# Optimization experiments

Measured on AMD Instinct MI355X. Metric: run time of the kernel, lower is better.

The kernel has to match this reference:

```python
import jax, jax.numpy as jnp
import numpy as np

N_NODES = 100_000
N_EDGES = 1_600_000
VOCAB = 10_000
NUM_GRAPHS = 512
D_EMB, D_HID, D_OUT = 64, 128, 64


def _sage_conv(h, src, dst, Wl, b, Wr, num_nodes):
    """PyG SAGEConv with mean aggregation: lin_l(mean_{j in N(i)} x_j) + lin_r(x_i)."""
    msgs = h[src]                                               # [E, D]
    agg = jax.ops.segment_sum(msgs, dst, num_segments=num_nodes)
    deg = jax.ops.segment_sum(jnp.ones((src.shape[0], 1), h.dtype), dst,
                              num_segments=num_nodes)
    agg = agg / jnp.maximum(deg, 1.0)                           # mean over neighbors
    return agg @ Wl + b + h @ Wr


def setup_inputs() -> dict:
    key = jax.random.key(0)
    ks = jax.random.split(key, 12)
    x = jax.random.randint(ks[0], (N_NODES,), 0, VOCAB)
    edge_index = jax.random.randint(ks[1], (2, N_EDGES), 0, N_NODES)
    batch = jnp.sort(jax.random.randint(ks[2], (N_NODES,), 0, NUM_GRAPHS))
    edge_attr = jax.random.uniform(ks[3], (N_EDGES, 1), dtype=jnp.float32)
    embed = jax.random.normal(ks[4], (VOCAB, D_EMB), dtype=jnp.float32) * 0.02
    W1l = jax.random.normal(ks[5], (D_EMB, D_HID), dtype=jnp.float32) / np.sqrt(D_EMB)
    b1 = jnp.zeros((D_HID,), jnp.float32)
    W1r = jax.random.normal(ks[6], (D_EMB, D_HID), dtype=jnp.float32) / np.sqrt(D_EMB)
    W2l = jax.random.normal(ks[7], (D_HID, D_OUT), dtype=jnp.float32) / np.sqrt(D_HID)
    b2 = jnp.zeros((D_OUT,), jnp.float32)
    W2r = jax.random.normal(ks[8], (D_HID, D_OUT), dtype=jnp.float32) / np.sqrt(D_HID)
    return {"x": x, "edge_index": edge_index, "batch": batch, "edge_attr": edge_attr,
            "embed": embed, "W1l": W1l, "b1": b1, "W1r": W1r,
            "W2l": W2l, "b2": b2, "W2r": W2r}


def reference(x, edge_index, batch, edge_attr, embed, W1l, b1, W1r, W2l, b2, W2r):
    # edge_attr is passed in the original forward but PyG SAGEConv ignores edge weights.
    src, dst = edge_index[0], edge_index[1]
    h = embed[x]                                                # [N, 64]
    h = jax.nn.relu(_sage_conv(h, src, dst, W1l, b1, W1r, N_NODES))  # [N, 128]
    h = _sage_conv(h, src, dst, W2l, b2, W2r, N_NODES)          # [N, 64]
    out = jax.ops.segment_max(h, batch, num_segments=NUM_GRAPHS)  # [G, 64]
    return out
```

## Files before the change

### kernel.cpp

```cpp
#include <hip/hip_runtime.h>
#include <cstdint>

#define NN 100000
#define NE 1600000
#define NG 512
#define NP 100032
#define VOCAB 10000
#define NBUK 256
#define BSZ 391
#define CAP 7680
#define TILE 2048

typedef unsigned short u16;
typedef u16      u16x8  __attribute__((ext_vector_type(8)));
typedef __bf16   bf16x8 __attribute__((ext_vector_type(8)));
typedef float    f32x4  __attribute__((ext_vector_type(4)));
typedef float    f32x2  __attribute__((ext_vector_type(2)));
typedef unsigned uint4v __attribute__((ext_vector_type(4)));

__device__ __forceinline__ u16 f2bf(float f) {
    unsigned u = __float_as_uint(f);
    unsigned r = ((u >> 16) & 1u) + 0x7FFFu;
    return (u16)((u + r) >> 16);
}
__device__ __forceinline__ float bf2f(u16 h) {
    return __uint_as_float(((unsigned)h) << 16);
}

__device__ __forceinline__ unsigned encF(float f) {
    unsigned s = __float_as_uint(f);
    return (s & 0x80000000u) ? ~s : (s | 0x80000000u);
}
__device__ __forceinline__ float decF(unsigned m) {
    unsigned s = (m & 0x80000000u) ? (m ^ 0x80000000u) : ~m;
    return __uint_as_float(s);
}

template <bool HI>
__device__ __forceinline__ void gather8(const int* __restrict__ csr, int beg, int end,
                                        const u16* __restrict__ table, int lane,
                                        f32x2 acc[4]) {
    const int sub = lane >> 3, g8 = (lane & 7) * 8;
    for (int base = beg; base < end; base += 64) {
        int n = min(64, end - base);
        int s = (lane < n) ? csr[base + lane] : 0;
        for (int c = 0; c * 8 < n; c += 2) {
            #pragma unroll
            for (int u = 0; u < 2; ++u) {
                int i = (c + u) * 8 + sub;
                int e = __shfl(s, i, 64);
                u16x8 v = {0, 0, 0, 0, 0, 0, 0, 0};
                if (i < n) {
                    int r = HI ? (e >> 17) : (e & 0x1FFFF);
                    v = *(const u16x8*)(table + (size_t)r * 64 + g8);
                }
                uint4v uv = __builtin_bit_cast(uint4v, v);
                #pragma unroll
                for (int k = 0; k < 4; ++k) {
                    f32x2 w;
                    w[0] = __uint_as_float(uv[k] << 16);
                    w[1] = __uint_as_float(uv[k] & 0xFFFF0000u);
                    acc[k] += w;
                }
            }
        }
    }
}

__device__ __forceinline__ float reduce_dim(const f32x2 acc[4], float* sT, int lane) {
    const int sub = lane >> 3, g8 = (lane & 7) * 8;
    #pragma unroll
    for (int k = 0; k < 4; ++k) {
        sT[sub * 72 + g8 + 2 * k]     = acc[k][0];
        sT[sub * 72 + g8 + 2 * k + 1] = acc[k][1];
    }
    float t = 0.0f;
    #pragma unroll
    for (int sg = 0; sg < 8; ++sg) t += sT[sg * 72 + lane];
    return t;
}

__device__ __forceinline__ void prepW_body(const float* __restrict__ Wa,
                                           const float* __restrict__ Wb,
                                           int mode, u16* __restrict__ Wpk, int idx) {
    int fid = idx >> 6, lane = idx & 63;
    int cT = fid >> 2, ks = fid & 3;
    int quad = lane >> 4, l16 = lane & 15;
    int n = cT * 16 + l16;
    u16x8 v;
    #pragma unroll
    for (int j = 0; j < 8; ++j) {
        int k = ks * 32 + quad * 8 + j;
        float f = (mode == 0) ? (k < 64 ? Wa[k * 128 + n] : Wb[(k - 64) * 128 + n])
                              : (n < 64 ? Wa[k * 64 + n] : Wb[k * 64 + (n - 64)]);
        v[j] = f2bf(f);
    }
    *(u16x8*)(Wpk + idx * 8) = v;
}

__global__ __launch_bounds__(256) void k_prep(
        const float* __restrict__ emb, u16* __restrict__ embB,
        const float* __restrict__ W1l, const float* __restrict__ W1r,
        u16* __restrict__ Wpk1,
        const float* __restrict__ W2l, const float* __restrict__ W2r,
        u16* __restrict__ Wpk2, unsigned* __restrict__ om,
        int* __restrict__ gcur) {
    int bid = blockIdx.x, t = threadIdx.x;
    if (bid < 2500) {
        int i = bid * 256 + t;
        if (i < VOCAB * 64) embB[i] = f2bf(emb[i]);
    } else if (bid < 2508) {
        prepW_body(W1l, W1r, 0, Wpk1, (bid - 2500) * 256 + t);
    } else if (bid < 2516) {
        prepW_body(W2l, W2r, 1, Wpk2, (bid - 2508) * 256 + t);
    } else if (bid < 2644) {
        int i = (bid - 2516) * 256 + t;
        if (i < NG * 64) om[i] = 0x007FFFFFu;
    } else {
        if (t < NBUK) gcur[t] = 0;
    }
}

__global__ __launch_bounds__(256) void k_bucket(const int* __restrict__ ei,
                                                int* __restrict__ gcur,
                                                unsigned* __restrict__ gbuf) {
    __shared__ int cnt[NBUK];
    __shared__ int start[NBUK];
    __shared__ int gbase[NBUK];
    __shared__ int wsum[4];
    __shared__ unsigned buf[TILE];
    __shared__ unsigned char bkt[TILE];
    const int t = threadIdx.x;
    const int e0 = blockIdx.x * (NE / 256);
    const int e1 = e0 + (NE / 256);
    for (int tb = e0; tb < e1; tb += TILE) {
        const int tc = min(TILE, e1 - tb);
        cnt[t] = 0;
        __syncthreads();
        unsigned ent[TILE / 256];
        unsigned char eb[TILE / 256];
        u16 rk[TILE / 256];
        int nm = 0;
        for (int i = t; i < tc; i += 256) {
            int dst = ei[NE + tb + i];
            int src = ei[tb + i];
            unsigned b = (unsigned)dst / BSZ;
            unsigned dl = (unsigned)dst - b * BSZ;
            ent[nm] = (dl << 17) | (unsigned)src;
            eb[nm] = (unsigned char)b;
            rk[nm] = (u16)atomicAdd(&cnt[b], 1);
            ++nm;
        }
        __syncthreads();
        {
            int c = cnt[t];
            int s = c;
            #pragma unroll
            for (int d = 1; d < 64; d <<= 1) {
                int v = __shfl_up(s, d, 64);
                if ((t & 63) >= d) s += v;
            }
            if ((t & 63) == 63) wsum[t >> 6] = s;
            __syncthreads();
            int pre = 0;
            #pragma unroll
            for (int w = 0; w < 4; ++w) pre += (w < (t >> 6)) ? wsum[w] : 0;
            start[t] = pre + s - c;
            gbase[t] = atomicAdd(&gcur[t], c);
        }
        __syncthreads();
        for (int k = 0; k < nm; ++k) {
            int pos = start[eb[k]] + rk[k];
            buf[pos] = ent[k];
            bkt[pos] = eb[k];
        }
        __syncthreads();
        for (int i = t; i < tc; i += 256) {
            unsigned b = bkt[i];
            gbuf[(size_t)b * CAP + gbase[b] + (i - start[b])] = buf[i];
        }
        __syncthreads();
    }
}

__global__ __launch_bounds__(512) void k_csr(const unsigned* __restrict__ gbuf,
                                             const int* __restrict__ gcur,
                                             const int* __restrict__ x,
                                             int* __restrict__ off,
                                             int* __restrict__ csr) {
    __shared__ int hist[BSZ];
    __shared__ int curL[BSZ];
    __shared__ int wsum[8];
    __shared__ int sred[8];
    const int b = blockIdx.x, t = threadIdx.x;
    if (t < BSZ) hist[t] = 0;
    __syncthreads();
    const int size = gcur[b];
    const unsigned* gb = gbuf + (size_t)b * CAP;
    for (int i = t; i < size; i += 512)
        atomicAdd(&hist[gb[i] >> 17], 1);
    {
        int v = (t < 256 && t < b) ? gcur[t] : 0;
        #pragma unroll
        for (int d = 32; d > 0; d >>= 1) v += __shfl_down(v, d, 64);
        if ((t & 63) == 0) sred[t >> 6] = v;
    }
    __syncthreads();
    const int gbase = sred[0] + sred[1] + sred[2] + sred[3];
    int h = (t < BSZ) ? hist[t] : 0;
    int s = h;
    #pragma unroll
    for (int d = 1; d < 64; d <<= 1) {
        int v = __shfl_up(s, d, 64);
        if ((t & 63) >= d) s += v;
    }
    if ((t & 63) == 63) wsum[t >> 6] = s;
    __syncthreads();
    int pre = 0;
    #pragma unroll
    for (int w = 0; w < 7; ++w) pre += (w < (t >> 6)) ? wsum[w] : 0;
    if (t < BSZ) {
        int ex = gbase + pre + s - h;
        curL[t] = ex;
        int g0 = b * BSZ;
        if (g0 + t <= NN) off[g0 + t] = ex;
    }
    __syncthreads();
    for (int i = t; i < size; i += 512) {
        unsigned ent = gb[i];
        int src = (int)(ent & 0x1FFFFu);
        int dl  = (int)(ent >> 17);
        int pos = atomicAdd(&curL[dl], 1);
        csr[pos] = src | (x[src] << 17);
    }
}

__global__ __launch_bounds__(256) void k_gather1(const int* __restrict__ off,
                                                 const int* __restrict__ csr,
                                                 const int* __restrict__ x,
                                                 const u16* __restrict__ embB,
                                                 u16* __restrict__ A1) {
    __shared__ float sT[4][576];
    int wv = threadIdx.x >> 6, lane = threadIdx.x & 63;
    for (int grp = blockIdx.x; grp * 4 < NN; grp += gridDim.x) {
        int wid = grp * 4 + wv;
        int beg = off[wid], end = off[wid + 1];
        f32x2 acc[4] = {{0.f, 0.f}, {0.f, 0.f}, {0.f, 0.f}, {0.f, 0.f}};
        gather8<true>(csr, beg, end, embB, lane, acc);
        float t = reduce_dim(acc, sT[wv], lane);
        A1[wid * 128 + lane] = f2bf(t / fmaxf((float)(end - beg), 1.0f));
        A1[wid * 128 + 64 + lane] = embB[x[wid] * 64 + lane];
    }
}

__global__ __launch_bounds__(256) void k_gemm12(
        const u16* __restrict__ A1, const u16* __restrict__ Wpk1,
        const u16* __restrict__ Wpk2, const float* __restrict__ b1,
        u16* __restrict__ P, u16* __restrict__ Q) {
    __shared__ __align__(16) u16 sH1[64][136];
    int w = threadIdx.x >> 6, lane = threadIdx.x & 63;
    int quad = lane >> 4, l16 = lane & 15;
    u16x8 bf1[2][4], bf2[2][4];
    #pragma unroll
    for (int ct = 0; ct < 2; ++ct)
        #pragma unroll
        for (int ks = 0; ks < 4; ++ks) {
            int fid = (w * 2 + ct) * 4 + ks;
            bf1[ct][ks] = *(const u16x8*)(Wpk1 + (fid * 64 + lane) * 8);
            bf2[ct][ks] = *(const u16x8*)(Wpk2 + (fid * 64 + lane) * 8);
        }
    int r0 = blockIdx.x * 64;
    #pragma unroll
    for (int rt = 0; rt < 4; ++rt) {
        int row = r0 + rt * 16 + l16;
        u16x8 a[4];
        #pragma unroll
        for (int ks = 0; ks < 4; ++ks)
            a[ks] = *(const u16x8*)(A1 + row * 128 + ks * 32 + quad * 8);
        #pragma unroll
        for (int ct = 0; ct < 2; ++ct) {
            f32x4 acc = {0.f, 0.f, 0.f, 0.f};
            #pragma unroll
            for (int ks = 0; ks < 4; ++ks)
                acc = __builtin_amdgcn_mfma_f32_16x16x32_bf16(
                    __builtin_bit_cast(bf16x8, a[ks]),
                    __builtin_bit_cast(bf16x8, bf1[ct][ks]), acc, 0, 0, 0);
            int col = w * 32 + ct * 16 + l16;
            float bias = b1[col];
            int lr = rt * 16 + quad * 4;
            #pragma unroll
            for (int reg = 0; reg < 4; ++reg)
                sH1[lr + reg][col] = f2bf(fmaxf(acc[reg] + bias, 0.f));
        }
    }
    __syncthreads();
    #pragma unroll
    for (int rt = 0; rt < 4; ++rt) {
        u16x8 a[4];
        #pragma unroll
        for (int ks = 0; ks < 4; ++ks)
            a[ks] = *(const u16x8*)(&sH1[rt * 16 + l16][ks * 32 + quad * 8]);
        #pragma unroll
        for (int ct = 0; ct < 2; ++ct) {
            f32x4 acc = {0.f, 0.f, 0.f, 0.f};
            #pragma unroll
            for (int ks = 0; ks < 4; ++ks)
                acc = __builtin_amdgcn_mfma_f32_16x16x32_bf16(
                    __builtin_bit_cast(bf16x8, a[ks]),
                    __builtin_bit_cast(bf16x8, bf2[ct][ks]), acc, 0, 0, 0);
            int col = w * 32 + ct * 16 + l16;
            int gr = r0 + rt * 16 + quad * 4;
            u16* dstT = (col < 64) ? P : Q;
            int c = col & 63;
            #pragma unroll
            for (int reg = 0; reg < 4; ++reg)
                dstT[(gr + reg) * 64 + c] = f2bf(acc[reg]);
        }
    }
}

__global__ __launch_bounds__(256) void k_final(const int* __restrict__ off,
                                               const int* __restrict__ csr,
                                               const u16* __restrict__ P,
                                               const u16* __restrict__ Q,
                                               const float* __restrict__ b2,
                                               const int* __restrict__ batch,
                                               unsigned* __restrict__ om) {
    __shared__ float sT[4][576];
    __shared__ float sR[4][64];
    __shared__ int sG[4];
    int wv = threadIdx.x >> 6, lane = threadIdx.x & 63;
    for (int grp = blockIdx.x; grp * 4 < NN; grp += gridDim.x) {
        int node = grp * 4 + wv;
        int beg = off[node], end = off[node + 1];
        f32x2 acc[4] = {{0.f, 0.f}, {0.f, 0.f}, {0.f, 0.f}, {0.f, 0.f}};
        gather8<false>(csr, beg, end, P, lane, acc);
        float t = reduce_dim(acc, sT[wv], lane);
        float r = t / fmaxf((float)(end - beg), 1.0f) + b2[lane]
                + bf2f(Q[node * 64 + lane]);
        int g = batch[node];
        sR[wv][lane] = r;
        if (lane == 0) sG[wv] = g;
        __syncthreads();
        bool leader = (wv == 0) || (sG[wv - 1] != g);
        if (leader) {
            float m = r;
            for (int u = wv + 1; u < 4 && sG[u] == g; ++u) m = fmaxf(m, sR[u][lane]);
            atomicMax(&om[g * 64 + lane], encF(m));
        }
        __syncthreads();
    }
}

__global__ void k_decode(const unsigned* __restrict__ om, float* __restrict__ out) {
    int i = blockIdx.x * blockDim.x + threadIdx.x;
    if (i < NG * 64) out[i] = decF(om[i]);
}

extern "C" void kernel_launch(void* const* d_in, const int* in_sizes, int n_in,
                              void* d_out, int out_size, void* d_ws, size_t ws_size,
                              hipStream_t stream) {
    const int*   x     = (const int*)d_in[0];
    const int*   ei    = (const int*)d_in[1];
    const int*   batch = (const int*)d_in[2];
    const float* emb   = (const float*)d_in[4];
    const float* W1l   = (const float*)d_in[5];
    const float* b1    = (const float*)d_in[6];
    const float* W1r   = (const float*)d_in[7];
    const float* W2l   = (const float*)d_in[8];
    const float* b2    = (const float*)d_in[9];
    const float* W2r   = (const float*)d_in[10];
    float* out = (float*)d_out;

    char* p = (char*)d_ws;
    u16* A1   = (u16*)p;               p += (size_t)NP * 128 * 2;
    u16* P    = (u16*)p;               p += (size_t)NP * 64 * 2;
    u16* Q    = (u16*)p;               p += (size_t)NP * 64 * 2;
    int* csr  = (int*)p;               p += (size_t)NE * 4;
    unsigned* gbuf = (unsigned*)p;     p += (size_t)NBUK * CAP * 4;
    int* gcur = (int*)p;               p += NBUK * 4;
    int* off  = (int*)p;               p += (size_t)(NN + 1) * 4;
    u16* Wpk1 = (u16*)p;               p += 16384 * 2;
    u16* Wpk2 = (u16*)p;               p += 16384 * 2;
    u16* embB = (u16*)p;               p += (size_t)VOCAB * 64 * 2;
    unsigned* om = (unsigned*)p;

    k_prep<<<2645, 256, 0, stream>>>(emb, embB, W1l, W1r, Wpk1, W2l, W2r, Wpk2,
                                     om, gcur);
    k_bucket<<<256, 256, 0, stream>>>(ei, gcur, gbuf);
    k_csr<<<NBUK, 512, 0, stream>>>(gbuf, gcur, x, off, csr);
    k_gather1<<<2048, 256, 0, stream>>>(off, csr, x, embB, A1);
    k_gemm12<<<NP / 64, 256, 0, stream>>>(A1, Wpk1, Wpk2, b1, P, Q);
    k_final<<<2048, 256, 0, stream>>>(off, csr, P, Q, b2, batch, om);
    k_decode<<<(NG * 64 + 255) / 256, 256, 0, stream>>>(om, out);
}
```

Before: 221.6 us.

## Fuse edge bucketing into prep kernel and neighbor gather into first GEMM

```diff
diff --git a/kernel.cpp b/kernel.cpp
--- a/kernel.cpp
+++ b/kernel.cpp
@@ -9,9 +9,10 @@
 #define NBUK 256
 #define BSZ 391
 #define CAP 7680
-#define TILE 2048
+#define EPB 1563
 
 typedef unsigned short u16;
+typedef u16      u16x4  __attribute__((ext_vector_type(4)));
 typedef u16      u16x8  __attribute__((ext_vector_type(8)));
 typedef __bf16   bf16x8 __attribute__((ext_vector_type(8)));
 typedef float    f32x4  __attribute__((ext_vector_type(4)));
@@ -98,88 +99,81 @@
     *(u16x8*)(Wpk + idx * 8) = v;
 }
 
-__global__ __launch_bounds__(256) void k_prep(
+__global__ __launch_bounds__(256) void k_fused(
+        const int* __restrict__ ei, int* __restrict__ gcur,
+        unsigned* __restrict__ gbuf,
         const float* __restrict__ emb, u16* __restrict__ embB,
         const float* __restrict__ W1l, const float* __restrict__ W1r,
         u16* __restrict__ Wpk1,
         const float* __restrict__ W2l, const float* __restrict__ W2r,
-        u16* __restrict__ Wpk2, unsigned* __restrict__ om,
-        int* __restrict__ gcur) {
-    int bid = blockIdx.x, t = threadIdx.x;
-    if (bid < 2500) {
-        int i = bid * 256 + t;
-        if (i < VOCAB * 64) embB[i] = f2bf(emb[i]);
-    } else if (bid < 2508) {
-        prepW_body(W1l, W1r, 0, Wpk1, (bid - 2500) * 256 + t);
-    } else if (bid < 2516) {
-        prepW_body(W2l, W2r, 1, Wpk2, (bid - 2508) * 256 + t);
-    } else if (bid < 2644) {
-        int i = (bid - 2516) * 256 + t;
-        if (i < NG * 64) om[i] = 0x007FFFFFu;
-    } else {
-        if (t < NBUK) gcur[t] = 0;
-    }
-}
-
-__global__ __launch_bounds__(256) void k_bucket(const int* __restrict__ ei,
-                                                int* __restrict__ gcur,
-                                                unsigned* __restrict__ gbuf) {
+        u16* __restrict__ Wpk2, unsigned* __restrict__ om) {
+    const int bid = blockIdx.x, t = threadIdx.x;
+    if (bid >= 1024) {
+        if (bid < 1649) {
+            int i = (bid - 1024) * 1024 + t * 4;
+            float4 f = *(const float4*)(emb + i);
+            u16x4 o = {f2bf(f.x), f2bf(f.y), f2bf(f.z), f2bf(f.w)};
+            *(u16x4*)(embB + i) = o;
+        } else if (bid < 1657) {
+            prepW_body(W1l, W1r, 0, Wpk1, (bid - 1649) * 256 + t);
+        } else if (bid < 1665) {
+            prepW_body(W2l, W2r, 1, Wpk2, (bid - 1657) * 256 + t);
+        } else {
+            om[(bid - 1665) * 256 + t] = 0x007FFFFFu;
+        }
+        return;
+    }
     __shared__ int cnt[NBUK];
     __shared__ int start[NBUK];
     __shared__ int gbase[NBUK];
     __shared__ int wsum[4];
-    __shared__ unsigned buf[TILE];
-    __shared__ unsigned char bkt[TILE];
-    const int t = threadIdx.x;
-    const int e0 = blockIdx.x * (NE / 256);
-    const int e1 = e0 + (NE / 256);
-    for (int tb = e0; tb < e1; tb += TILE) {
-        const int tc = min(TILE, e1 - tb);
-        cnt[t] = 0;
+    __shared__ unsigned buf[EPB];
+    __shared__ unsigned char bkt[EPB];
+    const int e0 = bid * EPB;
+    const int tc = min(NE - e0, EPB);
+    cnt[t] = 0;
+    __syncthreads();
+    unsigned ent[7];
+    unsigned char eb[7];
+    u16 rk[7];
+    int nm = 0;
+    for (int i = t; i < tc; i += 256) {
+        int dst = ei[NE + e0 + i];
+        int src = ei[e0 + i];
+        unsigned b = (unsigned)dst / BSZ;
+        unsigned dl = (unsigned)dst - b * BSZ;
+        ent[nm] = (dl << 17) | (unsigned)src;
+        eb[nm] = (unsigned char)b;
+        rk[nm] = (u16)atomicAdd(&cnt[b], 1);
+        ++nm;
+    }
+    __syncthreads();
+    {
+        int c = cnt[t];
+        int s = c;
+        #pragma unroll
+        for (int d = 1; d < 64; d <<= 1) {
+            int v = __shfl_up(s, d, 64);
+            if ((t & 63) >= d) s += v;
+        }
+        if ((t & 63) == 63) wsum[t >> 6] = s;
         __syncthreads();
-        unsigned ent[TILE / 256];
-        unsigned char eb[TILE / 256];
-        u16 rk[TILE / 256];
-        int nm = 0;
-        for (int i = t; i < tc; i += 256) {
-            int dst = ei[NE + tb + i];
-            int src = ei[tb + i];
-            unsigned b = (unsigned)dst / BSZ;
-            unsigned dl = (unsigned)dst - b * BSZ;
-            ent[nm] = (dl << 17) | (unsigned)src;
-            eb[nm] = (unsigned char)b;
-            rk[nm] = (u16)atomicAdd(&cnt[b], 1);
-            ++nm;
-        }
-        __syncthreads();
-        {
-            int c = cnt[t];
-            int s = c;
-            #pragma unroll
-            for (int d = 1; d < 64; d <<= 1) {
-                int v = __shfl_up(s, d, 64);
-                if ((t & 63) >= d) s += v;
-            }
-            if ((t & 63) == 63) wsum[t >> 6] = s;
-            __syncthreads();
-            int pre = 0;
-            #pragma unroll
-            for (int w = 0; w < 4; ++w) pre += (w < (t >> 6)) ? wsum[w] : 0;
-            start[t] = pre + s - c;
-            gbase[t] = atomicAdd(&gcur[t], c);
-        }
-        __syncthreads();
-        for (int k = 0; k < nm; ++k) {
-            int pos = start[eb[k]] + rk[k];
-            buf[pos] = ent[k];
-            bkt[pos] = eb[k];
-        }
-        __syncthreads();
-        for (int i = t; i < tc; i += 256) {
-            unsigned b = bkt[i];
-            gbuf[(size_t)b * CAP + gbase[b] + (i - start[b])] = buf[i];
-        }
-        __syncthreads();
+        int pre = 0;
+        #pragma unroll
+        for (int w = 0; w < 4; ++w) pre += (w < (t >> 6)) ? wsum[w] : 0;
+        start[t] = pre + s - c;
+        gbase[t] = atomicAdd(&gcur[t], c);
+    }
+    __syncthreads();
+    for (int k = 0; k < nm; ++k) {
+        int pos = start[eb[k]] + rk[k];
+        buf[pos] = ent[k];
+        bkt[pos] = eb[k];
+    }
+    __syncthreads();
+    for (int i = t; i < tc; i += 256) {
+        unsigned b = bkt[i];
+        gbuf[(size_t)b * CAP + gbase[b] + (i - start[b])] = buf[i];
     }
 }
 
@@ -235,48 +229,46 @@
     }
 }
 
-__global__ __launch_bounds__(256) void k_gather1(const int* __restrict__ off,
-                                                 const int* __restrict__ csr,
-                                                 const int* __restrict__ x,
-                                                 const u16* __restrict__ embB,
-                                                 u16* __restrict__ A1) {
-    __shared__ float sT[4][576];
-    int wv = threadIdx.x >> 6, lane = threadIdx.x & 63;
-    for (int grp = blockIdx.x; grp * 4 < NN; grp += gridDim.x) {
-        int wid = grp * 4 + wv;
-        int beg = off[wid], end = off[wid + 1];
-        f32x2 acc[4] = {{0.f, 0.f}, {0.f, 0.f}, {0.f, 0.f}, {0.f, 0.f}};
-        gather8<true>(csr, beg, end, embB, lane, acc);
-        float t = reduce_dim(acc, sT[wv], lane);
-        A1[wid * 128 + lane] = f2bf(t / fmaxf((float)(end - beg), 1.0f));
-        A1[wid * 128 + 64 + lane] = embB[x[wid] * 64 + lane];
-    }
-}
-
-__global__ __launch_bounds__(256) void k_gemm12(
-        const u16* __restrict__ A1, const u16* __restrict__ Wpk1,
-        const u16* __restrict__ Wpk2, const float* __restrict__ b1,
+__global__ __launch_bounds__(256) void k_gg(
+        const int* __restrict__ off, const int* __restrict__ csr,
+        const int* __restrict__ x, const u16* __restrict__ embB,
+        const u16* __restrict__ Wpk1, const u16* __restrict__ Wpk2,
+        const float* __restrict__ b1,
         u16* __restrict__ P, u16* __restrict__ Q) {
+    __shared__ __align__(16) u16 sA1[64][136];
     __shared__ __align__(16) u16 sH1[64][136];
-    int w = threadIdx.x >> 6, lane = threadIdx.x & 63;
-    int quad = lane >> 4, l16 = lane & 15;
-    u16x8 bf1[2][4], bf2[2][4];
+    const int wv = threadIdx.x >> 6, lane = threadIdx.x & 63;
+    const int quad = lane >> 4, l16 = lane & 15;
+    float* sT = (float*)&sH1[0][0] + wv * 576;
+    const int base = blockIdx.x * 64;
+    for (int it = 0; it < 16; ++it) {
+        int lr = wv * 16 + it;
+        int node = base + lr;
+        if (node < NN) {
+            int beg = off[node], end = off[node + 1];
+            f32x2 acc[4] = {{0.f, 0.f}, {0.f, 0.f}, {0.f, 0.f}, {0.f, 0.f}};
+            gather8<true>(csr, beg, end, embB, lane, acc);
+            float tv = reduce_dim(acc, sT, lane);
+            sA1[lr][lane] = f2bf(tv / fmaxf((float)(end - beg), 1.0f));
+            sA1[lr][64 + lane] = embB[x[node] * 64 + lane];
+        } else {
+            sA1[lr][lane] = 0;
+            sA1[lr][64 + lane] = 0;
+        }
+    }
+    __syncthreads();
+    u16x8 bf1[2][4];
     #pragma unroll
     for (int ct = 0; ct < 2; ++ct)
         #pragma unroll
-        for (int ks = 0; ks < 4; ++ks) {
-            int fid = (w * 2 + ct) * 4 + ks;
-            bf1[ct][ks] = *(const u16x8*)(Wpk1 + (fid * 64 + lane) * 8);
-            bf2[ct][ks] = *(const u16x8*)(Wpk2 + (fid * 64 + lane) * 8);
-        }
-    int r0 = blockIdx.x * 64;
+        for (int ks = 0; ks < 4; ++ks)
+            bf1[ct][ks] = *(const u16x8*)(Wpk1 + (((wv * 2 + ct) * 4 + ks) * 64 + lane) * 8);
     #pragma unroll
     for (int rt = 0; rt < 4; ++rt) {
-        int row = r0 + rt * 16 + l16;
         u16x8 a[4];
         #pragma unroll
         for (int ks = 0; ks < 4; ++ks)
-            a[ks] = *(const u16x8*)(A1 + row * 128 + ks * 32 + quad * 8);
+            a[ks] = *(const u16x8*)(&sA1[rt * 16 + l16][ks * 32 + quad * 8]);
         #pragma unroll
         for (int ct = 0; ct < 2; ++ct) {
             f32x4 acc = {0.f, 0.f, 0.f, 0.f};
@@ -285,7 +277,7 @@
                 acc = __builtin_amdgcn_mfma_f32_16x16x32_bf16(
                     __builtin_bit_cast(bf16x8, a[ks]),
                     __builtin_bit_cast(bf16x8, bf1[ct][ks]), acc, 0, 0, 0);
-            int col = w * 32 + ct * 16 + l16;
+            int col = wv * 32 + ct * 16 + l16;
             float bias = b1[col];
             int lr = rt * 16 + quad * 4;
             #pragma unroll
@@ -294,6 +286,12 @@
         }
     }
     __syncthreads();
+    u16x8 bf2[2][4];
+    #pragma unroll
+    for (int ct = 0; ct < 2; ++ct)
+        #pragma unroll
+        for (int ks = 0; ks < 4; ++ks)
+            bf2[ct][ks] = *(const u16x8*)(Wpk2 + (((wv * 2 + ct) * 4 + ks) * 64 + lane) * 8);
     #pragma unroll
     for (int rt = 0; rt < 4; ++rt) {
         u16x8 a[4];
@@ -308,8 +306,8 @@
                 acc = __builtin_amdgcn_mfma_f32_16x16x32_bf16(
                     __builtin_bit_cast(bf16x8, a[ks]),
                     __builtin_bit_cast(bf16x8, bf2[ct][ks]), acc, 0, 0, 0);
-            int col = w * 32 + ct * 16 + l16;
-            int gr = r0 + rt * 16 + quad * 4;
+            int col = wv * 32 + ct * 16 + l16;
+            int gr = base + rt * 16 + quad * 4;
             u16* dstT = (col < 64) ? P : Q;
             int c = col & 63;
             #pragma unroll
@@ -373,7 +371,6 @@
     float* out = (float*)d_out;
 
     char* p = (char*)d_ws;
-    u16* A1   = (u16*)p;               p += (size_t)NP * 128 * 2;
     u16* P    = (u16*)p;               p += (size_t)NP * 64 * 2;
     u16* Q    = (u16*)p;               p += (size_t)NP * 64 * 2;
     int* csr  = (int*)p;               p += (size_t)NE * 4;
@@ -385,12 +382,11 @@
     u16* embB = (u16*)p;               p += (size_t)VOCAB * 64 * 2;
     unsigned* om = (unsigned*)p;
 
-    k_prep<<<2645, 256, 0, stream>>>(emb, embB, W1l, W1r, Wpk1, W2l, W2r, Wpk2,
-                                     om, gcur);
-    k_bucket<<<256, 256, 0, stream>>>(ei, gcur, gbuf);
+    hipMemsetAsync(gcur, 0, sizeof(int) * NBUK, stream);
+    k_fused<<<1793, 256, 0, stream>>>(ei, gcur, gbuf, emb, embB,
+                                      W1l, W1r, Wpk1, W2l, W2r, Wpk2, om);
     k_csr<<<NBUK, 512, 0, stream>>>(gbuf, gcur, x, off, csr);
-    k_gather1<<<2048, 256, 0, stream>>>(off, csr, x, embB, A1);
-    k_gemm12<<<NP / 64, 256, 0, stream>>>(A1, Wpk1, Wpk2, b1, P, Q);
+    k_gg<<<NP / 64, 256, 0, stream>>>(off, csr, x, embB, Wpk1, Wpk2, b1, P, Q);
     k_final<<<2048, 256, 0, stream>>>(off, csr, P, Q, b2, batch, om);
     k_decode<<<(NG * 64 + 255) / 256, 256, 0, stream>>>(om, out);
 }
```

New measurement: 225.3 us. Within noise of the previous version (+1.7%).
